# Kernel tuning notes

Measured on AMD Instinct MI355X. Metric: run time of the kernel, lower is better.

The kernel has to match this reference:

```python
import jax, jax.numpy as jnp
import numpy as np

T, B, D, H = 256, 256, 512, 1024


def setup_inputs() -> dict:
    key = jax.random.key(0)
    ks = jax.random.split(key, 9)
    s = 0.02  # small init scale for numerical sanity
    return {
        "inputs": jax.random.normal(ks[0], (T, B, D), dtype=jnp.float32),
        "Wf": jax.random.normal(ks[1], (D + H, H), dtype=jnp.float32) * s,
        "bf": jax.random.normal(ks[2], (H,), dtype=jnp.float32) * s,
        "Wi": jax.random.normal(ks[3], (D + H, H), dtype=jnp.float32) * s,
        "bi": jax.random.normal(ks[4], (H,), dtype=jnp.float32) * s,
        "Wg": jax.random.normal(ks[5], (D + H, H), dtype=jnp.float32) * s,
        "bg": jax.random.normal(ks[6], (H,), dtype=jnp.float32) * s,
        "Wo": jax.random.normal(ks[7], (D + H, H), dtype=jnp.float32) * s,
        "bo": jax.random.normal(ks[8], (H,), dtype=jnp.float32) * s,
    }


def reference(inputs, Wf, bf, Wi, bi, Wg, bg, Wo, bo):
    hidden_dim = Wf.shape[1]
    batch = inputs.shape[1]
    # Fuse the four gate projections into one [D+H, 4H] GEMM per step.
    W = jnp.concatenate([Wf, Wi, Wg, Wo], axis=1)   # [D+H, 4H]
    b = jnp.concatenate([bf, bi, bg, bo], axis=0)   # [4H]

    h0 = jnp.zeros((batch, hidden_dim), dtype=inputs.dtype)
    c0 = jnp.zeros((batch, hidden_dim), dtype=inputs.dtype)

    def step(carry, x):
        hx, cx = carry
        combined = jnp.concatenate([x, hx], axis=1)  # [B, D+H]
        z = combined @ W + b                          # [B, 4H]
        f, i, g, o = jnp.split(z, 4, axis=1)
        f = jax.nn.sigmoid(f)
        i = jax.nn.sigmoid(i)
        g = jnp.tanh(g)
        o = jax.nn.sigmoid(o)
        cx = f * cx + i * g
        hx = o * jnp.tanh(cx)
        return (hx, cx), hx

    (hx, cx), outputs = jax.lax.scan(step, (h0, c0), inputs)
    return outputs, hx, cx
```

## Files before the change

kernel.cpp:

```cpp
#include <hip/hip_runtime.h>
#include <cstdint>
#include <cstddef>

#define T_STEPS 256
#define BATCH   256
#define DIN     512
#define HID     1024
#define KTOT    1536
#define NOUT    4096
#define BHSZ    ((size_t)BATCH * HID)

typedef __bf16 bf16;
typedef __bf16 bf16x4 __attribute__((ext_vector_type(4)));
typedef __bf16 bf16x8 __attribute__((ext_vector_type(8)));
typedef float  f32x4  __attribute__((ext_vector_type(4)));

__device__ __forceinline__ void store_bf16_sc(bf16* p, bf16 v) {
  unsigned short u = __builtin_bit_cast(unsigned short, v);
  asm volatile("global_store_short %0, %1, off sc0 sc1" :: "v"(p), "v"(u) : "memory");
}

#define VMW_(N) asm volatile("s_waitcnt vmcnt(" #N ")" ::: "memory")
#define VMW(N) do { VMW_(N); __builtin_amdgcn_sched_barrier(0); } while (0)
#define LGKM0() do { asm volatile("s_waitcnt lgkmcnt(0)" ::: "memory"); \
                     __builtin_amdgcn_sched_barrier(0); } while (0)
#define SBAR() __builtin_amdgcn_sched_barrier(0)
#define RAWBAR() do { SBAR(); __builtin_amdgcn_s_barrier(); SBAR(); } while (0)

__device__ __forceinline__ float fexp2(float x) {
  float r; asm("v_exp_f32 %0, %1" : "=v"(r) : "v"(x)); return r;
}
__device__ __forceinline__ float frcp(float x) {
  float r; asm("v_rcp_f32 %0, %1" : "=v"(r) : "v"(x)); return r;
}
__device__ __forceinline__ float fsigmoid(float x) {
  return frcp(1.f + fexp2(-1.44269504f * x));
}
__device__ __forceinline__ float ftanh(float x) {
  return 1.f - 2.f * frcp(1.f + fexp2(2.88539008f * x));
}

__global__ void convert_w_kernel(const float* __restrict__ Wf, const float* __restrict__ Wi,
                                 const float* __restrict__ Wg, const float* __restrict__ Wo,
                                 bf16* __restrict__ Wt) {
  __shared__ float tile[64][17];
  const int k0 = blockIdx.x * 64;
  const int jb = blockIdx.y;
  const int j0 = jb * 16;
  const int t  = threadIdx.x;
  const float* srcs[4] = {Wf, Wi, Wg, Wo};
#pragma unroll
  for (int g = 0; g < 4; ++g) {
    const float* src = srcs[g];
    {
      const int jl = t & 15, kb = t >> 4;
#pragma unroll
      for (int r = 0; r < 4; ++r) {
        const int kl = kb + 16 * r;
        tile[kl][jl] = src[(size_t)(k0 + kl) * HID + (j0 + jl)];
      }
    }
    __syncthreads();
    {
      const int kk = t & 63, jl4 = t >> 6;
#pragma unroll
      for (int r = 0; r < 4; ++r) {
        const int jl = jl4 + 4 * r;
        Wt[(size_t)(jb * 64 + g * 16 + jl) * KTOT + (k0 + kk)] = (bf16)tile[kk][jl];
      }
    }
    __syncthreads();
  }
}

__global__ void convert_x_kernel(const float* __restrict__ X, bf16* __restrict__ xb) {
  const int t = blockIdx.y;
  const int i = blockIdx.x * blockDim.x + threadIdx.x;
  const float4 v = ((const float4*)(X + (size_t)t * BATCH * DIN))[i];
  bf16x4 o;
  o[0] = (bf16)v.x; o[1] = (bf16)v.y; o[2] = (bf16)v.z; o[3] = (bf16)v.w;
  ((bf16x4*)(xb + (size_t)t * BATCH * DIN))[i] = o;
}

__global__ __launch_bounds__(512, 2)
void lstm_v11(const bf16* __restrict__ Bt,
              const bf16* __restrict__ xb,
              bf16* __restrict__ hseq,
              const bf16* __restrict__ zb16,
              float* __restrict__ outF,
              const float* __restrict__ bf_, const float* __restrict__ bi_,
              const float* __restrict__ bg_, const float* __restrict__ bo_,
              unsigned* __restrict__ flags) {
  __shared__ f32x4 redu[8][16][64];

  const int tid = threadIdx.x, lane = tid & 63, wid = tid >> 6;
  const int bid = blockIdx.x;
  const int e8  = bid & 7;
  const int mblk = e8 >> 1;
  const int nblk = ((bid >> 3) << 1) | (e8 & 1);
  const int bm0 = mblk * 64;
  const int bn0 = nblk * 64;
  const int fr = lane & 15, fq = lane >> 4;

  if (tid == 0)
    (void)__hip_atomic_load(flags, __ATOMIC_ACQUIRE, __HIP_MEMORY_SCOPE_AGENT);
  __syncthreads();

  const int j = nblk * 16 + fr;
  const float bfv = bf_[j], biv = bi_[j], bgv = bg_[j], bov = bo_[j];
  float cr[2] = {0.f, 0.f};

  bf16x8 breg[6][4];
#pragma unroll
  for (int s = 0; s < 6; ++s) {
    const int ks = wid + 8 * s;
#pragma unroll
    for (int nf = 0; nf < 4; ++nf)
      breg[s][nf] = *(const bf16x8*)(Bt + (size_t)(bn0 + nf * 16 + fr) * KTOT
                                     + ks * 32 + fq * 8);
  }

  bf16x8 S0[4], S1[4], S2[4], S3[4];

  auto ldx = [&](int t2, int s, bf16x8 (&slot)[4]) {
    const bf16* src = xb + (size_t)t2 * BATCH * DIN + (wid + 8 * s) * 32 + fq * 8;
#pragma unroll
    for (int mf = 0; mf < 4; ++mf)
      slot[mf] = *(const bf16x8*)(src + (size_t)(bm0 + mf * 16 + fr) * DIN);
  };
  auto ldh = [&](int t2, int s, bf16x8 (&slot)[4]) {
    const bf16* base = (t2 == 0) ? zb16 : hseq + (size_t)(t2 - 1) * BHSZ;
    const bf16* src = base + (wid + 8 * s) * 32 - 512 + fq * 8;
#pragma unroll
    for (int mf = 0; mf < 4; ++mf)
      slot[mf] = *(const bf16x8*)(src + (size_t)(bm0 + mf * 16 + fr) * HID);
  };

  const int pn8 = 2 * wid + ((lane & 7) >> 1) * 16 + (lane & 1);
  auto poll = [&](int tprev) {
    const unsigned* f = flags + (size_t)tprev * 256 + mblk * 64 + pn8;
    const unsigned long long tt0 = __builtin_amdgcn_s_memrealtime();
    for (;;) {
      unsigned v = __hip_atomic_load(f, __ATOMIC_RELAXED,
                                     __HIP_MEMORY_SCOPE_AGENT);
      if (__all(v != 0)) break;
      __builtin_amdgcn_s_sleep(1);
      if (__builtin_amdgcn_s_memrealtime() - tt0 > (1ULL << 22)) break;
    }
    asm volatile("" ::: "memory");
    __builtin_amdgcn_sched_barrier(0);
  };

#define MFMA16(ACC, SLOT, S) do {                                           \
    __builtin_amdgcn_s_setprio(1);                                          \
    _Pragma("unroll")                                                       \
    for (int mf_ = 0; mf_ < 4; ++mf_) {                                     \
      _Pragma("unroll")                                                     \
      for (int nf_ = 0; nf_ < 4; ++nf_)                                     \
        ACC[mf_][nf_] = __builtin_amdgcn_mfma_f32_16x16x32_bf16(            \
            SLOT[mf_], breg[S][nf_], ACC[mf_][nf_], 0, 0, 0);               \
    }                                                                       \
    __builtin_amdgcn_s_setprio(0);                                          \
  } while (0)

#define STEP(T0, XA, XB, HA, HB, HC, HD, NA, NB) do {                       \
    const int t_ = (T0);                                                    \
    f32x4 acc[4][4] = {};                                                   \
    VMW(4);  MFMA16(acc, XA, 0);                                            \
    VMW(0);  MFMA16(acc, XB, 1);                                            \
    if (t_ > 0) poll(t_ - 1);                    \
    ldh(t_, 2, HA); ldh(t_, 3, HB); ldh(t_, 4, HC); ldh(t_, 5, HD); SBAR(); \
    VMW(12); MFMA16(acc, HA, 2);                                            \
    VMW(8);  MFMA16(acc, HB, 3);                                            \
    VMW(4);  MFMA16(acc, HC, 4);                                            \
    VMW(0);  MFMA16(acc, HD, 5);                                            \
            \
    _Pragma("unroll")                                                       \
    for (int mf_ = 0; mf_ < 4; ++mf_) {                                     \
      _Pragma("unroll")                                                     \
      for (int nf_ = 0; nf_ < 4; ++nf_)                                     \
        redu[wid][mf_ * 4 + nf_][lane] = acc[mf_][nf_];                     \
    }                                                                       \
    LGKM0();                                                                \
    RAWBAR();                             \
    const int fbase_ = (wid >> 1) * 4;                                      \
    const int rh_ = wid & 1;                                                \
    float z_[2][4];                                                         \
    _Pragma("unroll")                                                       \
    for (int e_ = 0; e_ < 2; ++e_) {                                        \
      const int rloc_ = rh_ * 8 + fq * 2 + e_;                              \
      const int lsel_ = (rloc_ >> 2) * 16 + fr;                             \
      const int rc_ = rloc_ & 3;                                            \
      _Pragma("unroll")                                                     \
      for (int nf_ = 0; nf_ < 4; ++nf_) {                                   \
        float sum_ = 0.f;                                                   \
        _Pragma("unroll")                                                   \
        for (int s_ = 0; s_ < 8; ++s_)                                      \
          sum_ += ((const float*)&redu[s_][fbase_ + nf_][lsel_])[rc_];      \
        z_[e_][nf_] = sum_;                                                 \
      }                                                                     \
    }                                                                       \
    float* outSl_ = outF + (size_t)t_ * BHSZ;                               \
    _Pragma("unroll")                                                       \
    for (int e_ = 0; e_ < 2; ++e_) {                                        \
      const float fg_ = fsigmoid(z_[e_][0] + bfv);                          \
      const float ig_ = fsigmoid(z_[e_][1] + biv);                          \
      const float gg_ = ftanh(z_[e_][2] + bgv);                             \
      const float og_ = fsigmoid(z_[e_][3] + bov);                          \
      cr[e_] = fg_ * cr[e_] + ig_ * gg_;                                    \
      const float h_ = og_ * ftanh(cr[e_]);                                 \
      const int m_ = bm0 + wid * 8 + fq * 2 + e_;                           \
      const size_t off_ = (size_t)m_ * HID + j;                             \
      outSl_[off_] = h_;                                                    \
      store_bf16_sc(hseq + (size_t)t_ * BHSZ + off_, (bf16)h_);             \
      if (t_ == T_STEPS - 1)                                                \
        outF[(size_t)(T_STEPS + 1) * BHSZ + off_] = cr[e_];                 \
    }                                                                       \
    if (t_ + 1 < T_STEPS) {                                                 \
      ldx(t_ + 1, 0, NA); ldx(t_ + 1, 1, NB); SBAR();                       \
      VMW(8);              \
    } else {                                                                \
      VMW(0);                                                               \
    }                                                                       \
    RAWBAR();           \
    if (tid == 0)                                                           \
      __hip_atomic_store(&flags[(size_t)t_ * 256 + mblk * 64 + nblk], 1u,   \
                         __ATOMIC_RELAXED, __HIP_MEMORY_SCOPE_AGENT);       \
  } while (0)

  ldx(0, 0, S0); SBAR();
  ldx(0, 1, S1); SBAR();

#pragma unroll 1
  for (int t = 0; t < T_STEPS; t += 2) {
    STEP(t,     S0, S1, S2, S3, S0, S1, S2, S3);
    STEP(t + 1, S2, S3, S0, S1, S2, S3, S0, S1);
  }
#undef STEP
#undef MFMA16
}

__global__ __launch_bounds__(512, 2)
void lstm_fb(const bf16* __restrict__ Bt,
             const float* __restrict__ X,
             const float* __restrict__ zbF,
             float* __restrict__ outF,
             const float* __restrict__ bf_, const float* __restrict__ bi_,
             const float* __restrict__ bg_, const float* __restrict__ bo_,
             unsigned* __restrict__ flags) {
  __shared__ f32x4 redu[8][16][64];
  const int tid = threadIdx.x, lane = tid & 63, wid = tid >> 6;
  const int bid = blockIdx.x;
  const int xcd = bid & 7, sl = bid >> 3;
  const int nblk = xcd * 8 + (sl & 7);
  const int mblk = sl >> 3;
  const int bm0 = mblk * 64;
  const int bn0 = nblk * 64;
  const int fr = lane & 15, fq = lane >> 4;

  if (tid == 0)
    (void)__hip_atomic_load(flags, __ATOMIC_ACQUIRE, __HIP_MEMORY_SCOPE_AGENT);
  __syncthreads();

  const int j = nblk * 16 + fr;
  const float bfv = bf_[j], biv = bi_[j], bgv = bg_[j], bov = bo_[j];
  float cr[2] = {0.f, 0.f};

  bf16x8 breg[6][4];
#pragma unroll
  for (int s = 0; s < 6; ++s) {
    const int ks = wid + 8 * s;
#pragma unroll
    for (int nf = 0; nf < 4; ++nf)
      breg[s][nf] = *(const bf16x8*)(Bt + (size_t)(bn0 + nf * 16 + fr) * KTOT
                                     + ks * 32 + fq * 8);
  }

  bf16x8 afp[2][4];

  auto poll = [&](int tprev) {
    const unsigned* f = flags + (size_t)tprev * 256 + mblk * 64;
    const unsigned long long tt0 = __builtin_amdgcn_s_memrealtime();
    for (;;) {
      unsigned v = __hip_atomic_load(f + lane, __ATOMIC_RELAXED,
                                     __HIP_MEMORY_SCOPE_AGENT);
      if (__all(v != 0)) break;
      __builtin_amdgcn_s_sleep(2);
      if (__builtin_amdgcn_s_memrealtime() - tt0 > (1ULL << 22)) break;
    }
    asm volatile("" ::: "memory");
    __builtin_amdgcn_sched_barrier(0);
  };

  auto loadA = [&](int t2, int s, int p) __attribute__((always_inline)) {
    const int ks = wid + 8 * s;
    const int k = ks * 32 + fq * 8;
    if (s == 2 && t2 > 0) poll(t2 - 1);
    const float* src; int ld, kk;
    if (s < 2) { src = X + (size_t)t2 * BATCH * DIN; ld = DIN; kk = k; }
    else {
      src = (t2 == 0) ? zbF : outF + (size_t)(t2 - 1) * BHSZ;
      ld = HID; kk = k - 512;
    }
#pragma unroll
    for (int mf = 0; mf < 4; ++mf) {
      const float* q = src + (size_t)(bm0 + mf * 16 + fr) * ld + kk;
      const f32x4 lo = *(const f32x4*)q;
      const f32x4 hi = *(const f32x4*)(q + 4);
      bf16x8 v;
      v[0] = (bf16)lo[0]; v[1] = (bf16)lo[1]; v[2] = (bf16)lo[2]; v[3] = (bf16)lo[3];
      v[4] = (bf16)hi[0]; v[5] = (bf16)hi[1]; v[6] = (bf16)hi[2]; v[7] = (bf16)hi[3];
      afp[p][mf] = v;
    }
  };

  loadA(0, 0, 0);

#pragma unroll 1
  for (int t = 0; t < T_STEPS; ++t) {
    f32x4 acc[4][4] = {};
#pragma unroll
    for (int s = 0; s < 6; ++s) {
      if (s < 5)                loadA(t, s + 1, (s + 1) & 1);
      else if (t + 1 < T_STEPS) loadA(t + 1, 0, 0);
      __builtin_amdgcn_s_setprio(1);
#pragma unroll
      for (int mf = 0; mf < 4; ++mf)
#pragma unroll
        for (int nf = 0; nf < 4; ++nf)
          acc[mf][nf] = __builtin_amdgcn_mfma_f32_16x16x32_bf16(
              afp[s & 1][mf], breg[s][nf], acc[mf][nf], 0, 0, 0);
      __builtin_amdgcn_s_setprio(0);
    }

#pragma unroll
    for (int mf = 0; mf < 4; ++mf)
#pragma unroll
      for (int nf = 0; nf < 4; ++nf)
        redu[wid][mf * 4 + nf][lane] = acc[mf][nf];
    __syncthreads();

    const int fbase = (wid >> 1) * 4;
    const int rh = wid & 1;
    float z[2][4];
#pragma unroll
    for (int e = 0; e < 2; ++e) {
      const int rloc = rh * 8 + fq * 2 + e;
      const int lsel = (rloc >> 2) * 16 + fr;
      const int rc = rloc & 3;
#pragma unroll
      for (int nf = 0; nf < 4; ++nf) {
        float sum = 0.f;
#pragma unroll
        for (int s = 0; s < 8; ++s)
          sum += ((const float*)&redu[s][fbase + nf][lsel])[rc];
        z[e][nf] = sum;
      }
    }

    float* outSl = outF + (size_t)t * BHSZ;
#pragma unroll
    for (int e = 0; e < 2; ++e) {
      const float fg = 1.f / (1.f + expf(-(z[e][0] + bfv)));
      const float ig = 1.f / (1.f + expf(-(z[e][1] + biv)));
      const float gg = tanhf(z[e][2] + bgv);
      const float og = 1.f / (1.f + expf(-(z[e][3] + bov)));
      cr[e] = fg * cr[e] + ig * gg;
      const float h = og * tanhf(cr[e]);
      const int m = bm0 + wid * 8 + fq * 2 + e;
      const size_t off = (size_t)m * HID + j;
      __hip_atomic_store(&outSl[off], h, __ATOMIC_RELAXED,
                         __HIP_MEMORY_SCOPE_AGENT);
      if (t == T_STEPS - 1)
        outF[(size_t)(T_STEPS + 1) * BHSZ + off] = cr[e];
    }
    asm volatile("s_waitcnt vmcnt(0)" ::: "memory");
    __syncthreads();
    if (tid == 0)
      __hip_atomic_store(&flags[(size_t)t * 256 + mblk * 64 + nblk], 1u,
                         __ATOMIC_RELAXED, __HIP_MEMORY_SCOPE_AGENT);
  }
}

extern "C" void kernel_launch(void* const* d_in, const int* in_sizes, int n_in,
                              void* d_out, int out_size, void* d_ws, size_t ws_size,
                              hipStream_t stream) {
  const float* X   = (const float*)d_in[0];
  const float* Wf  = (const float*)d_in[1];
  const float* bf_ = (const float*)d_in[2];
  const float* Wi  = (const float*)d_in[3];
  const float* bi_ = (const float*)d_in[4];
  const float* Wg  = (const float*)d_in[5];
  const float* bg_ = (const float*)d_in[6];
  const float* Wo  = (const float*)d_in[7];
  const float* bo_ = (const float*)d_in[8];
  float* out = (float*)d_out;

  const size_t WtB   = (size_t)NOUT * KTOT * 2;
  const size_t zBb   = BHSZ * 4;
  const size_t flagB = (size_t)T_STEPS * 256 * 4;
  const size_t XbB   = (size_t)T_STEPS * BATCH * DIN * 2;
  const size_t HsB   = (size_t)T_STEPS * BHSZ * 2;

  char* ws = (char*)d_ws;
  bf16*     Wt    = (bf16*)ws;              ws += WtB;
  float*    zbF   = (float*)(void*)ws;      ws += zBb;
  unsigned* flags = (unsigned*)(void*)ws;   ws += flagB;

  const bool big = ws_size >= WtB + zBb + flagB + XbB + HsB + (1u << 20);
  bf16* xbp = nullptr;  bf16* hseq = nullptr;
  if (big) {
    xbp  = (bf16*)ws;   ws += XbB;
    hseq = (bf16*)ws;
  }

  hipMemsetAsync(zbF, 0, zBb + flagB, stream);

  convert_w_kernel<<<dim3(KTOT / 64, NOUT / 64), 256, 0, stream>>>(Wf, Wi, Wg, Wo, Wt);

  if (big) {
    convert_x_kernel<<<dim3(BATCH * DIN / 4 / 256, T_STEPS), 256, 0, stream>>>(X, xbp);
    lstm_v11<<<256, 512, 0, stream>>>(Wt, xbp, hseq, (const bf16*)zbF, out,
                                      bf_, bi_, bg_, bo_, flags);
  } else {
    lstm_fb<<<256, 512, 0, stream>>>(Wt, X, zbF, out,
                                     bf_, bi_, bg_, bo_, flags);
  }

  hipMemcpyAsync(out + (size_t)T_STEPS * BHSZ, out + (size_t)(T_STEPS - 1) * BHSZ,
                 BHSZ * 4, hipMemcpyDeviceToDevice, stream);
}
```

Before: 2.259 ms.

## Store bf16 hidden state in per-block tiled layout for coalesced exchange

Changes the bf16 hidden-state exchange buffer from row-major [B,H] to 64x16 tiles ordered by (mblk, column block). Each workgroup now writes its h tile as contiguous 128-byte runs per wave, and consumers load 16-column chunks from contiguous tiles. The aim is fewer partial cache lines on the latency-critical cross-block h store and reload path. The reduction mapping is rearranged so each lane produces rows matching the new tile order, and the outstanding-load wait count is adjusted to match.

```diff
diff --git a/kernel.cpp b/kernel.cpp
--- a/kernel.cpp
+++ b/kernel.cpp
@@ -83,7 +83,7 @@
 }
 
 __global__ __launch_bounds__(512, 2)
-void lstm_v11(const bf16* __restrict__ Bt,
+void lstm_v12(const bf16* __restrict__ Bt,
               const bf16* __restrict__ xb,
               bf16* __restrict__ hseq,
               const bf16* __restrict__ zb16,
@@ -129,11 +129,15 @@
       slot[mf] = *(const bf16x8*)(src + (size_t)(bm0 + mf * 16 + fr) * DIN);
   };
   auto ldh = [&](int t2, int s, bf16x8 (&slot)[4]) {
-    const bf16* base = (t2 == 0) ? zb16 : hseq + (size_t)(t2 - 1) * BHSZ;
-    const bf16* src = base + (wid + 8 * s) * 32 - 512 + fq * 8;
+    const int c0 = (wid + 8 * s) * 32 - 512;
+    const int pp = (c0 >> 4) + (fq >> 1);
+    const bf16* base = (t2 == 0)
+        ? zb16
+        : hseq + (((size_t)(t2 - 1) << 8) + mblk * 64 + pp) * 1024;
+    const int coloff = (fq & 1) * 8;
 #pragma unroll
     for (int mf = 0; mf < 4; ++mf)
-      slot[mf] = *(const bf16x8*)(src + (size_t)(bm0 + mf * 16 + fr) * HID);
+      slot[mf] = *(const bf16x8*)(base + (mf * 16 + fr) * 16 + coloff);
   };
 
   const int pn8 = 2 * wid + ((lane & 7) >> 1) * 16 + (lane & 1);
@@ -174,7 +178,7 @@
     VMW(8);  MFMA16(acc, HB, 3);                                            \
     VMW(4);  MFMA16(acc, HC, 4);                                            \
     VMW(0);  MFMA16(acc, HD, 5);                                            \
-            \
+                      \
     _Pragma("unroll")                                                       \
     for (int mf_ = 0; mf_ < 4; ++mf_) {                                     \
       _Pragma("unroll")                                                     \
@@ -182,47 +186,48 @@
         redu[wid][mf_ * 4 + nf_][lane] = acc[mf_][nf_];                     \
     }                                                                       \
     LGKM0();                                                                \
-    RAWBAR();                             \
-    const int fbase_ = (wid >> 1) * 4;                                      \
-    const int rh_ = wid & 1;                                                \
-    float z_[2][4];                                                         \
+    RAWBAR();                                                               \
+    const int mfo_ = wid >> 1;                                              \
+    float hv_[2];                                                           \
     _Pragma("unroll")                                                       \
     for (int e_ = 0; e_ < 2; ++e_) {                                        \
-      const int rloc_ = rh_ * 8 + fq * 2 + e_;                              \
-      const int lsel_ = (rloc_ >> 2) * 16 + fr;                             \
-      const int rc_ = rloc_ & 3;                                            \
+         \
+      const int lsel_ = (((wid & 1) << 1) + e_) * 16 + fr;                  \
+      float z_[4];                                                          \
       _Pragma("unroll")                                                     \
       for (int nf_ = 0; nf_ < 4; ++nf_) {                                   \
         float sum_ = 0.f;                                                   \
         _Pragma("unroll")                                                   \
         for (int s_ = 0; s_ < 8; ++s_)                                      \
-          sum_ += ((const float*)&redu[s_][fbase_ + nf_][lsel_])[rc_];      \
-        z_[e_][nf_] = sum_;                                                 \
+          sum_ += ((const float*)&redu[s_][mfo_ * 4 + nf_][lsel_])[fq];     \
+        z_[nf_] = sum_;                                                     \
       }                                                                     \
+      const float fg_ = fsigmoid(z_[0] + bfv);                              \
+      const float ig_ = fsigmoid(z_[1] + biv);                              \
+      const float gg_ = ftanh(z_[2] + bgv);                                 \
+      const float og_ = fsigmoid(z_[3] + bov);                              \
+      cr[e_] = fg_ * cr[e_] + ig_ * gg_;                                    \
+      hv_[e_] = og_ * ftanh(cr[e_]);                                        \
     }                                                                       \
+           \
+    bf16* tile_ = hseq + (((size_t)t_ << 8) + mblk * 64 + nblk) * 1024;     \
+    store_bf16_sc(&tile_[wid * 128 + lane], (bf16)hv_[0]);                  \
+    store_bf16_sc(&tile_[wid * 128 + 64 + lane], (bf16)hv_[1]);             \
     float* outSl_ = outF + (size_t)t_ * BHSZ;                               \
     _Pragma("unroll")                                                       \
     for (int e_ = 0; e_ < 2; ++e_) {                                        \
-      const float fg_ = fsigmoid(z_[e_][0] + bfv);                          \
-      const float ig_ = fsigmoid(z_[e_][1] + biv);                          \
-      const float gg_ = ftanh(z_[e_][2] + bgv);                             \
-      const float og_ = fsigmoid(z_[e_][3] + bov);                          \
-      cr[e_] = fg_ * cr[e_] + ig_ * gg_;                                    \
-      const float h_ = og_ * ftanh(cr[e_]);                                 \
-      const int m_ = bm0 + wid * 8 + fq * 2 + e_;                           \
-      const size_t off_ = (size_t)m_ * HID + j;                             \
-      outSl_[off_] = h_;                                                    \
-      store_bf16_sc(hseq + (size_t)t_ * BHSZ + off_, (bf16)h_);             \
+      const size_t off_ = (size_t)(bm0 + wid * 8 + e_ * 4 + fq) * HID + j;  \
+      outSl_[off_] = hv_[e_];                                               \
       if (t_ == T_STEPS - 1)                                                \
         outF[(size_t)(T_STEPS + 1) * BHSZ + off_] = cr[e_];                 \
     }                                                                       \
     if (t_ + 1 < T_STEPS) {                                                 \
       ldx(t_ + 1, 0, NA); ldx(t_ + 1, 1, NB); SBAR();                       \
-      VMW(8);              \
+      VMW(10);         \
     } else {                                                                \
       VMW(0);                                                               \
     }                                                                       \
-    RAWBAR();           \
+    RAWBAR();                                                               \
     if (tid == 0)                                                           \
       __hip_atomic_store(&flags[(size_t)t_ * 256 + mblk * 64 + nblk], 1u,   \
                          __ATOMIC_RELAXED, __HIP_MEMORY_SCOPE_AGENT);       \
@@ -400,7 +405,7 @@
   const size_t zBb   = BHSZ * 4;
   const size_t flagB = (size_t)T_STEPS * 256 * 4;
   const size_t XbB   = (size_t)T_STEPS * BATCH * DIN * 2;
-  const size_t HsB   = (size_t)T_STEPS * BHSZ * 2;
+  const size_t HsB   = (size_t)T_STEPS * 256 * 1024 * 2;
 
   char* ws = (char*)d_ws;
   bf16*     Wt    = (bf16*)ws;              ws += WtB;
@@ -420,7 +425,7 @@
 
   if (big) {
     convert_x_kernel<<<dim3(BATCH * DIN / 4 / 256, T_STEPS), 256, 0, stream>>>(X, xbp);
-    lstm_v11<<<256, 512, 0, stream>>>(Wt, xbp, hseq, (const bf16*)zbF, out,
+    lstm_v12<<<256, 512, 0, stream>>>(Wt, xbp, hseq, (const bf16*)zbF, out,
                                       bf_, bi_, bg_, bo_, flags);
   } else {
     lstm_fb<<<256, 512, 0, stream>>>(Wt, X, zbF, out,
```

Result: faster. 2.062 ms (-8.7%).
